# Performance work log

Hardware: AMD Instinct MI355X
Metric: run time of the kernel (lower is better)

## Reference

```python
import jax, jax.numpy as jnp
import numpy as np

EPS = 1e-6
B, N, K = 4, 65536, 16
D_IN, D_OUT, DH = 8, 16, 8  # DH = d_out // 2


def _bn(x, g, b):
    # train-mode BatchNorm2d over (B, N, K) per channel (channels-last here)
    m = jnp.mean(x, axis=(0, 1, 2))
    v = jnp.var(x, axis=(0, 1, 2))
    return (x - m) * jax.lax.rsqrt(v + EPS) * g + b


def _conv(x, w, b):
    # 1x1 Conv2d == per-point linear; x: (B,N,K,Cin), w: (Cout,Cin)
    return jnp.einsum('bnki,oi->bnko', x, w) + b


def _lse(coords, feats, idx, w, b, g, bt):
    # coords: (B,N,3), feats: (B,N,1,D), idx: (B,N,K)
    nbrs = jnp.take_along_axis(coords[:, :, None, :], idx[:, :, :, None], axis=1)  # (B,N,K,3)
    ctr = jnp.broadcast_to(coords[:, :, None, :], nbrs.shape)
    dist = jnp.ones(idx.shape + (1,), dtype=coords.dtype)  # torch path passes idx only -> dist = ones
    enc = jnp.concatenate([ctr, nbrs, ctr - nbrs, dist], axis=-1)  # (B,N,K,10)
    h = jax.nn.relu(_bn(_conv(enc, w, b), g, bt))
    f = jnp.broadcast_to(feats, idx.shape + (feats.shape[-1],))
    return jnp.concatenate([h, f], axis=-1)  # (B,N,K,2*D)


def _pool(x, sw, w, b, g, bt):
    # attentive pooling: softmax over neighbor axis K (axis=2)
    scores = jax.nn.softmax(jnp.einsum('bnki,oi->bnko', x, sw), axis=2)
    agg = jnp.sum(scores * x, axis=2, keepdims=True)  # (B,N,1,C)
    return jax.nn.relu(_bn(_conv(agg, w, b), g, bt))


def setup_inputs() -> dict:
    key = jax.random.key(0)
    ks = jax.random.split(key, 16)
    rn = lambda k, s: (0.1 * jax.random.normal(k, s)).astype(jnp.float32)
    inp = {
        'coords': jax.random.normal(ks[0], (B, N, 3), dtype=jnp.float32),
        'features': jax.random.normal(ks[1], (B, D_IN, N, 1), dtype=jnp.float32),
        'idx': jax.random.randint(ks[2], (B, N, K), 0, N, dtype=jnp.int32),
        # mlp1: d_in -> d_out//2, no bn, LeakyReLU(0.2)
        'w1': rn(ks[3], (DH, D_IN)), 'b1': jnp.zeros((DH,), jnp.float32),
        # lse1 mlp: 10 -> d_out//2, bn + ReLU
        'lse1_w': rn(ks[4], (DH, 10)), 'lse1_b': jnp.zeros((DH,), jnp.float32),
        'lse1_g': jnp.ones((DH,), jnp.float32), 'lse1_bt': jnp.zeros((DH,), jnp.float32),
        # pool1: in d_out -> out d_out//2
        'p1_sw': rn(ks[5], (D_OUT, D_OUT)),
        'p1_w': rn(ks[6], (DH, D_OUT)), 'p1_b': jnp.zeros((DH,), jnp.float32),
        'p1_g': jnp.ones((DH,), jnp.float32), 'p1_bt': jnp.zeros((DH,), jnp.float32),
        # lse2
        'lse2_w': rn(ks[7], (DH, 10)), 'lse2_b': jnp.zeros((DH,), jnp.float32),
        'lse2_g': jnp.ones((DH,), jnp.float32), 'lse2_bt': jnp.zeros((DH,), jnp.float32),
        # pool2: in d_out -> out d_out
        'p2_sw': rn(ks[8], (D_OUT, D_OUT)),
        'p2_w': rn(ks[9], (D_OUT, D_OUT)), 'p2_b': jnp.zeros((D_OUT,), jnp.float32),
        'p2_g': jnp.ones((D_OUT,), jnp.float32), 'p2_bt': jnp.zeros((D_OUT,), jnp.float32),
        # mlp2: d_out -> 2*d_out (no bn/act)
        'w2': rn(ks[10], (2 * D_OUT, D_OUT)), 'b2': jnp.zeros((2 * D_OUT,), jnp.float32),
        # shortcut: d_in -> 2*d_out, bn, no act
        'sc_w': rn(ks[11], (2 * D_OUT, D_IN)), 'sc_b': jnp.zeros((2 * D_OUT,), jnp.float32),
        'sc_g': jnp.ones((2 * D_OUT,), jnp.float32), 'sc_bt': jnp.zeros((2 * D_OUT,), jnp.float32),
    }
    return inp


def reference(coords, features, idx, w1, b1, lse1_w, lse1_b, lse1_g, lse1_bt,
              p1_sw, p1_w, p1_b, p1_g, p1_bt, lse2_w, lse2_b, lse2_g, lse2_bt,
              p2_sw, p2_w, p2_b, p2_g, p2_bt, w2, b2, sc_w, sc_b, sc_g, sc_bt):
    feats = jnp.transpose(features, (0, 2, 3, 1))  # (B,N,1,d_in) channels-last
    x = jax.nn.leaky_relu(_conv(feats, w1, b1), 0.2)           # (B,N,1,DH)
    x = _lse(coords, x, idx, lse1_w, lse1_b, lse1_g, lse1_bt)  # (B,N,K,D_OUT)
    x = _pool(x, p1_sw, p1_w, p1_b, p1_g, p1_bt)               # (B,N,1,DH)
    x = _lse(coords, x, idx, lse2_w, lse2_b, lse2_g, lse2_bt)  # (B,N,K,D_OUT)
    x = _pool(x, p2_sw, p2_w, p2_b, p2_g, p2_bt)               # (B,N,1,D_OUT)
    out = jax.nn.leaky_relu(
        _conv(x, w2, b2) + _bn(_conv(feats, sc_w, sc_b), sc_g, sc_bt), 0.01)
    return jnp.transpose(out, (0, 3, 1, 2))  # (B, 2*d_out, N, 1)
```

## Files before the change

kernel.cpp:

```cpp
#include <hip/hip_runtime.h>

#define NB 4
#define NN 65536
#define NK 16
#define NP (NB * NN)
#define BN_EPS 1e-6f
#define LOG2E 1.44269504088896f

#define WS_ENC_M   0
#define WS_SC_M    32
#define WS_S_Y2    96
#define WS_SS_Y2   104
#define WS_S_Y4    112
#define WS_SS_Y4   128
#define WS_Y2      1024
#define WS_Y4      (1024 + NP * 8)
#define WS_C4      (1024 + NP * 24)

template <int NCH>
__device__ inline void blockReduceAtomic(float (&v)[NCH], float* __restrict__ dst) {
    __shared__ float red[4][NCH];
    const int lane = threadIdx.x & 63;
    const int wv = threadIdx.x >> 6;
    __syncthreads();
#pragma unroll
    for (int c = 0; c < NCH; c++) {
        float x = v[c];
#pragma unroll
        for (int off = 32; off > 0; off >>= 1) x += __shfl_xor(x, off, 64);
        if (lane == 0) red[wv][c] = x;
    }
    __syncthreads();
    for (int c = threadIdx.x; c < NCH; c += 256)
        atomicAdd(dst + c, red[0][c] + red[1][c] + red[2][c] + red[3][c]);
    __syncthreads();
}

__device__ inline void bn_from_enc(const float* __restrict__ M, const float* __restrict__ w,
                                   float b, float g, float bt, float& sc, float& sh) {
    float u[6];
    u[0] = w[0] + w[6]; u[1] = w[1] + w[7]; u[2] = w[2] + w[8];
    u[3] = w[3] - w[6]; u[4] = w[4] - w[7]; u[5] = w[5] - w[8];
    const float beta = b + w[9];
    float lin = 0.f;
#pragma unroll
    for (int i = 0; i < 6; i++) lin += u[i] * M[i];
    float quad = u[0] * u[0] * M[6] + 2.f * u[0] * u[1] * M[7] + 2.f * u[0] * u[2] * M[8]
               + u[1] * u[1] * M[9] + 2.f * u[1] * u[2] * M[10] + u[2] * u[2] * M[11];
#pragma unroll
    for (int i = 0; i < 3; i++)
#pragma unroll
        for (int j = 0; j < 3; j++) quad += 2.f * u[i] * u[3 + j] * M[12 + i * 3 + j];
    quad += u[3] * u[3] * M[21] + 2.f * u[3] * u[4] * M[22] + 2.f * u[3] * u[5] * M[23]
          + u[4] * u[4] * M[24] + 2.f * u[4] * u[5] * M[25] + u[5] * u[5] * M[26];
    const float cnt = (float)NP * (float)NK;
    const float sum = lin + cnt * beta;
    const float ss = quad + 2.f * beta * lin + cnt * beta * beta;
    const float m = sum / cnt, v = ss / cnt - m * m;
    sc = g * rsqrtf(v + BN_EPS);
    sh = bt - m * sc;
}

__global__ __launch_bounds__(256) void k_prep(
    const float* __restrict__ coords, float4* __restrict__ c4) {
    const int p = blockIdx.x * 256 + threadIdx.x;
    c4[p] = make_float4(coords[3 * p], coords[3 * p + 1], coords[3 * p + 2], 0.f);
}

__global__ __launch_bounds__(256) void k_stats(
    const float4* __restrict__ c4, const float* __restrict__ feats,
    const int* __restrict__ idx, float* __restrict__ ws) {
    const int tid = threadIdx.x;
    const int p = blockIdx.x * 256 + tid;
    const int b = p >> 16;
    const int n = p & (NN - 1);

    {
        float accf[44];
        float f[8];
#pragma unroll
        for (int i = 0; i < 8; i++) f[i] = feats[(b * 8 + i) * NN + n];
#pragma unroll
        for (int i = 0; i < 8; i++) accf[i] = f[i];
        int t2 = 8;
#pragma unroll
        for (int i = 0; i < 8; i++)
#pragma unroll
            for (int j = i; j < 8; j++) accf[t2++] = f[i] * f[j];
        blockReduceAtomic<44>(accf, ws + WS_SC_M);
    }

    const int boff = b << 16;
    const float4 me = c4[p];
    const int4* ip = (const int4*)idx + p * 4;
    float sn0 = 0.f, sn1 = 0.f, sn2 = 0.f;
    float m00 = 0.f, m01 = 0.f, m02 = 0.f, m11 = 0.f, m12 = 0.f, m22 = 0.f;
#pragma unroll
    for (int q = 0; q < 4; q++) {
        int4 v = ip[q];
        int jj[4] = {v.x, v.y, v.z, v.w};
#pragma unroll
        for (int e = 0; e < 4; e++) {
            const float4 nn = c4[boff + jj[e]];
            sn0 += nn.x; sn1 += nn.y; sn2 += nn.z;
            m00 += nn.x * nn.x; m01 += nn.x * nn.y; m02 += nn.x * nn.z;
            m11 += nn.y * nn.y; m12 += nn.y * nn.z; m22 += nn.z * nn.z;
        }
    }
    float acc[27];
    acc[0] = 16.f * me.x; acc[1] = 16.f * me.y; acc[2] = 16.f * me.z;
    acc[3] = sn0; acc[4] = sn1; acc[5] = sn2;
    acc[6] = 16.f * me.x * me.x; acc[7] = 16.f * me.x * me.y; acc[8] = 16.f * me.x * me.z;
    acc[9] = 16.f * me.y * me.y; acc[10] = 16.f * me.y * me.z; acc[11] = 16.f * me.z * me.z;
    acc[12] = me.x * sn0; acc[13] = me.x * sn1; acc[14] = me.x * sn2;
    acc[15] = me.y * sn0; acc[16] = me.y * sn1; acc[17] = me.y * sn2;
    acc[18] = me.z * sn0; acc[19] = me.z * sn1; acc[20] = me.z * sn2;
    acc[21] = m00; acc[22] = m01; acc[23] = m02;
    acc[24] = m11; acc[25] = m12; acc[26] = m22;
    blockReduceAtomic<27>(acc, ws + WS_ENC_M);
}

__global__ __launch_bounds__(256) void k_pool1(
    const float4* __restrict__ c4, const float* __restrict__ feats,
    const int* __restrict__ idx,
    const float* __restrict__ w1, const float* __restrict__ b1,
    const float* __restrict__ lse1_w, const float* __restrict__ lse1_b,
    const float* __restrict__ lse1_g, const float* __restrict__ lse1_bt,
    const float* __restrict__ p1_sw, const float* __restrict__ p1_w,
    const float* __restrict__ p1_b, float* __restrict__ ws) {
    __shared__ float an[24], dc3[24], dcon[8], sws[64], pws[128], pbs[8], w1s[64], b1s[8];
    const int tid = threadIdx.x;
    if (tid < 8) {
        const int c = tid;
        const float* w = lse1_w + c * 10;
        float sc, sh;
        bn_from_enc(ws + WS_ENC_M, w, lse1_b[c], lse1_g[c], lse1_bt[c], sc, sh);
#pragma unroll
        for (int i = 0; i < 3; i++) {
            an[c * 3 + i] = sc * (w[3 + i] - w[6 + i]);
            dc3[c * 3 + i] = sc * (w[i] + w[6 + i]);
        }
        dcon[c] = sc * (lse1_b[c] + w[9]) + sh;
        b1s[c] = b1[c]; pbs[c] = p1_b[c];
    }
    if (tid < 64) {
        w1s[tid] = w1[tid];
        sws[tid] = p1_sw[(tid >> 3) * 16 + (tid & 7)] * LOG2E;
    }
    if (tid < 128) pws[tid] = p1_w[tid];
    __syncthreads();

    const int p = blockIdx.x * 256 + tid;
    const int b = p >> 16;
    const int n = p & (NN - 1);
    const int boff = b << 16;
    const float4 me = c4[p];
    float d[8];
#pragma unroll
    for (int c = 0; c < 8; c++)
        d[c] = dc3[c * 3] * me.x + dc3[c * 3 + 1] * me.y + dc3[c * 3 + 2] * me.z + dcon[c];
    const int4* ip = (const int4*)idx + p * 4;
    float l[8] = {}, ac[8] = {};
#pragma unroll
    for (int q = 0; q < 4; q++) {
        int4 v = ip[q];
        int jj[4] = {v.x, v.y, v.z, v.w};
#pragma unroll
        for (int e = 0; e < 4; e++) {
            const float4 nn = c4[boff + jj[e]];
            float h[8];
#pragma unroll
            for (int c = 0; c < 8; c++) {
                float y = an[c * 3] * nn.x + an[c * 3 + 1] * nn.y + an[c * 3 + 2] * nn.z + d[c];
                h[c] = y > 0.f ? y : 0.f;
            }
#pragma unroll
            for (int o = 0; o < 8; o++) {
                float s = 0.f;
#pragma unroll
                for (int i = 0; i < 8; i++) s += h[i] * sws[o * 8 + i];
                float e2 = exp2f(s);
                l[o] += e2; ac[o] += e2 * h[o];
            }
        }
    }
    float f[8];
#pragma unroll
    for (int i = 0; i < 8; i++) f[i] = feats[(b * 8 + i) * NN + n];
    float agg[16];
#pragma unroll
    for (int o = 0; o < 8; o++) agg[o] = ac[o] / l[o];
#pragma unroll
    for (int jq = 0; jq < 8; jq++) {
        float y = b1s[jq];
#pragma unroll
        for (int i = 0; i < 8; i++) y += f[i] * w1s[jq * 8 + i];
        agg[8 + jq] = y > 0.f ? y : 0.2f * y;
    }
    float st[16];
#pragma unroll
    for (int c = 0; c < 8; c++) {
        float y = pbs[c];
#pragma unroll
        for (int o = 0; o < 16; o++) y += agg[o] * pws[c * 16 + o];
        ws[WS_Y2 + c * NP + p] = y;
        st[c] = y; st[8 + c] = y * y;
    }
    blockReduceAtomic<16>(st, ws + WS_S_Y2);
}

__global__ __launch_bounds__(256) void k_pool2(
    const float4* __restrict__ c4, const int* __restrict__ idx,
    const float* __restrict__ lse2_w, const float* __restrict__ lse2_b,
    const float* __restrict__ lse2_g, const float* __restrict__ lse2_bt,
    const float* __restrict__ p1_g, const float* __restrict__ p1_bt,
    const float* __restrict__ p2_sw, const float* __restrict__ p2_w,
    const float* __restrict__ p2_b, float* __restrict__ ws) {
    __shared__ float an[24], dc3[24], dcon[8], p1sc[8], p1sh[8], sws[64], pws[256], pbs[16];
    const int tid = threadIdx.x;
    if (tid < 8) {
        const int c = tid;
        const float* w = lse2_w + c * 10;
        float sc, sh;
        bn_from_enc(ws + WS_ENC_M, w, lse2_b[c], lse2_g[c], lse2_bt[c], sc, sh);
#pragma unroll
        for (int i = 0; i < 3; i++) {
            an[c * 3 + i] = sc * (w[3 + i] - w[6 + i]);
            dc3[c * 3 + i] = sc * (w[i] + w[6 + i]);
        }
        dcon[c] = sc * (lse2_b[c] + w[9]) + sh;
    } else if (tid < 16) {
        const int c = tid - 8;
        const float cP = 1.f / (float)NP;
        float m = ws[WS_S_Y2 + c] * cP, vv = ws[WS_SS_Y2 + c] * cP - m * m;
        float sc = p1_g[c] * rsqrtf(vv + BN_EPS);
        p1sc[c] = sc; p1sh[c] = p1_bt[c] - m * sc;
    }
    if (tid < 64) sws[tid] = p2_sw[(tid >> 3) * 16 + (tid & 7)] * LOG2E;
    if (tid < 256) pws[tid] = p2_w[tid];
    if (tid < 16) pbs[tid] = p2_b[tid];
    __syncthreads();

    const int p = blockIdx.x * 256 + tid;
    const int boff = (p >> 16) << 16;
    const float4 me = c4[p];
    float d[8];
#pragma unroll
    for (int c = 0; c < 8; c++)
        d[c] = dc3[c * 3] * me.x + dc3[c * 3 + 1] * me.y + dc3[c * 3 + 2] * me.z + dcon[c];
    const int4* ip = (const int4*)idx + p * 4;
    float l[8] = {}, ac[8] = {};
#pragma unroll
    for (int q = 0; q < 4; q++) {
        int4 v = ip[q];
        int jj[4] = {v.x, v.y, v.z, v.w};
#pragma unroll
        for (int e = 0; e < 4; e++) {
            const float4 nn = c4[boff + jj[e]];
            float h[8];
#pragma unroll
            for (int c = 0; c < 8; c++) {
                float y = an[c * 3] * nn.x + an[c * 3 + 1] * nn.y + an[c * 3 + 2] * nn.z + d[c];
                h[c] = y > 0.f ? y : 0.f;
            }
#pragma unroll
            for (int o = 0; o < 8; o++) {
                float s = 0.f;
#pragma unroll
                for (int i = 0; i < 8; i++) s += h[i] * sws[o * 8 + i];
                float e2 = exp2f(s);
                l[o] += e2; ac[o] += e2 * h[o];
            }
        }
    }
    float agg[16];
#pragma unroll
    for (int o = 0; o < 8; o++) agg[o] = ac[o] / l[o];
#pragma unroll
    for (int c = 0; c < 8; c++) {
        float y = ws[WS_Y2 + c * NP + p] * p1sc[c] + p1sh[c];
        agg[8 + c] = y > 0.f ? y : 0.f;
    }
    float st[32];
#pragma unroll
    for (int c = 0; c < 16; c++) {
        float y = pbs[c];
#pragma unroll
        for (int o = 0; o < 16; o++) y += agg[o] * pws[c * 16 + o];
        ws[WS_Y4 + c * NP + p] = y;
        st[c] = y; st[16 + c] = y * y;
    }
    blockReduceAtomic<32>(st, ws + WS_S_Y4);
}

__global__ __launch_bounds__(256) void k_final(
    const float* __restrict__ feats, const float* __restrict__ w2,
    const float* __restrict__ b2, const float* __restrict__ sc_w,
    const float* __restrict__ sc_b, const float* __restrict__ p2_g,
    const float* __restrict__ p2_bt, const float* __restrict__ sc_g,
    const float* __restrict__ sc_bt, const float* __restrict__ ws,
    float* __restrict__ out) {
    __shared__ float w2s[512], b2s[32], scws[256], scbs[32],
        p2sc[16], p2sh[16], scsc[32], scsh[32];
    const int tid = threadIdx.x;
    for (int i = tid; i < 512; i += 256) w2s[i] = w2[i];
    if (tid < 256) scws[tid] = sc_w[tid];
    if (tid < 32) {
        b2s[tid] = b2[tid]; scbs[tid] = sc_b[tid];
        const int c = tid;
        const float* w = sc_w + c * 8;
        const float* S = ws + WS_SC_M;
        float lin = 0.f;
#pragma unroll
        for (int i = 0; i < 8; i++) lin += w[i] * S[i];
        float quad = 0.f;
        int t2 = 0;
#pragma unroll
        for (int i = 0; i < 8; i++)
#pragma unroll
            for (int j = i; j < 8; j++) {
                const float mm = S[8 + t2++];
                quad += (i == j ? 1.f : 2.f) * w[i] * w[j] * mm;
            }
        const float cnt = (float)NP;
        const float bb = sc_b[c];
        const float sum = lin + cnt * bb;
        const float ss = quad + 2.f * bb * lin + cnt * bb * bb;
        const float m = sum / cnt, vv = ss / cnt - m * m;
        const float sc = sc_g[c] * rsqrtf(vv + BN_EPS);
        scsc[c] = sc; scsh[c] = sc_bt[c] - m * sc;
    }
    if (tid < 16) {
        const int c = tid;
        const float cP = 1.f / (float)NP;
        float m = ws[WS_S_Y4 + c] * cP, vv = ws[WS_SS_Y4 + c] * cP - m * m;
        float sc = p2_g[c] * rsqrtf(vv + BN_EPS);
        p2sc[c] = sc; p2sh[c] = p2_bt[c] - m * sc;
    }
    __syncthreads();

    const int p = blockIdx.x * 256 + tid;
    const int b = p >> 16;
    const int n = p & (NN - 1);
    float x4[16];
#pragma unroll
    for (int c = 0; c < 16; c++) {
        float y = ws[WS_Y4 + c * NP + p] * p2sc[c] + p2sh[c];
        x4[c] = y > 0.f ? y : 0.f;
    }
    float f[8];
#pragma unroll
    for (int i = 0; i < 8; i++) f[i] = feats[(b * 8 + i) * NN + n];
#pragma unroll
    for (int c = 0; c < 32; c++) {
        float s = scbs[c];
#pragma unroll
        for (int i = 0; i < 8; i++) s += f[i] * scws[c * 8 + i];
        s = s * scsc[c] + scsh[c];
        float m = b2s[c];
#pragma unroll
        for (int o = 0; o < 16; o++) m += x4[o] * w2s[c * 16 + o];
        float vv = m + s;
        out[(b * 32 + c) * NN + n] = vv > 0.f ? vv : 0.01f * vv;
    }
}

extern "C" void kernel_launch(void* const* d_in, const int* in_sizes, int n_in,
                              void* d_out, int out_size, void* d_ws, size_t ws_size,
                              hipStream_t stream) {
    (void)in_sizes; (void)n_in; (void)out_size; (void)ws_size;
    const float* coords = (const float*)d_in[0];
    const float* features = (const float*)d_in[1];
    const int* idx = (const int*)d_in[2];
    const float* w1 = (const float*)d_in[3];
    const float* b1 = (const float*)d_in[4];
    const float* lse1_w = (const float*)d_in[5];
    const float* lse1_b = (const float*)d_in[6];
    const float* lse1_g = (const float*)d_in[7];
    const float* lse1_bt = (const float*)d_in[8];
    const float* p1_sw = (const float*)d_in[9];
    const float* p1_w = (const float*)d_in[10];
    const float* p1_b = (const float*)d_in[11];
    const float* p1_g = (const float*)d_in[12];
    const float* p1_bt = (const float*)d_in[13];
    const float* lse2_w = (const float*)d_in[14];
    const float* lse2_b = (const float*)d_in[15];
    const float* lse2_g = (const float*)d_in[16];
    const float* lse2_bt = (const float*)d_in[17];
    const float* p2_sw = (const float*)d_in[18];
    const float* p2_w = (const float*)d_in[19];
    const float* p2_b = (const float*)d_in[20];
    const float* p2_g = (const float*)d_in[21];
    const float* p2_bt = (const float*)d_in[22];
    const float* w2 = (const float*)d_in[23];
    const float* b2 = (const float*)d_in[24];
    const float* sc_w = (const float*)d_in[25];
    const float* sc_b = (const float*)d_in[26];
    const float* sc_g = (const float*)d_in[27];
    const float* sc_bt = (const float*)d_in[28];
    float* ws = (float*)d_ws;
    float* out = (float*)d_out;
    float4* c4 = (float4*)(ws + WS_C4);

    const int NBLK = NP / 256;
    hipMemsetAsync(ws, 0, 144 * sizeof(float), stream);
    k_prep<<<NBLK, 256, 0, stream>>>(coords, c4);
    k_stats<<<NBLK, 256, 0, stream>>>(c4, features, idx, ws);
    k_pool1<<<NBLK, 256, 0, stream>>>(c4, features, idx, w1, b1, lse1_w, lse1_b,
                                      lse1_g, lse1_bt, p1_sw, p1_w, p1_b, ws);
    k_pool2<<<NBLK, 256, 0, stream>>>(c4, idx, lse2_w, lse2_b, lse2_g, lse2_bt,
                                      p1_g, p1_bt, p2_sw, p2_w, p2_b, ws);
    k_final<<<NBLK, 256, 0, stream>>>(features, w2, b2, sc_w, sc_b, p2_g, p2_bt,
                                      sc_g, sc_bt, ws, out);
}
```

Baseline: 363.9 us.

## Fuse both LSE/pool gathers into one pass and fold prep into stats

```diff
diff --git a/kernel.cpp b/kernel.cpp
--- a/kernel.cpp
+++ b/kernel.cpp
@@ -61,15 +61,9 @@
     sh = bt - m * sc;
 }
 
-__global__ __launch_bounds__(256) void k_prep(
-    const float* __restrict__ coords, float4* __restrict__ c4) {
-    const int p = blockIdx.x * 256 + threadIdx.x;
-    c4[p] = make_float4(coords[3 * p], coords[3 * p + 1], coords[3 * p + 2], 0.f);
-}
-
 __global__ __launch_bounds__(256) void k_stats(
-    const float4* __restrict__ c4, const float* __restrict__ feats,
-    const int* __restrict__ idx, float* __restrict__ ws) {
+    const float* __restrict__ coords, const float* __restrict__ feats,
+    const int* __restrict__ idx, float4* __restrict__ c4, float* __restrict__ ws) {
     const int tid = threadIdx.x;
     const int p = blockIdx.x * 256 + tid;
     const int b = p >> 16;
@@ -90,31 +84,53 @@
         blockReduceAtomic<44>(accf, ws + WS_SC_M);
     }
 
-    const int boff = b << 16;
-    const float4 me = c4[p];
+    const float cx = coords[3 * p], cy = coords[3 * p + 1], cz = coords[3 * p + 2];
+    c4[p] = make_float4(cx, cy, cz, 0.f);
+    const float* cb = coords + b * NN * 3;
     const int4* ip = (const int4*)idx + p * 4;
     float sn0 = 0.f, sn1 = 0.f, sn2 = 0.f;
     float m00 = 0.f, m01 = 0.f, m02 = 0.f, m11 = 0.f, m12 = 0.f, m22 = 0.f;
-#pragma unroll
-    for (int q = 0; q < 4; q++) {
-        int4 v = ip[q];
-        int jj[4] = {v.x, v.y, v.z, v.w};
+
+    auto proc = [&](float nx, float ny, float nz) {
+        sn0 += nx; sn1 += ny; sn2 += nz;
+        m00 += nx * nx; m01 += nx * ny; m02 += nx * nz;
+        m11 += ny * ny; m12 += ny * nz; m22 += nz * nz;
+    };
+
+    int4 v0 = ip[0];
+    float ax[4], ay[4], az[4];
+    {
+        int jj[4] = {v0.x, v0.y, v0.z, v0.w};
 #pragma unroll
         for (int e = 0; e < 4; e++) {
-            const float4 nn = c4[boff + jj[e]];
-            sn0 += nn.x; sn1 += nn.y; sn2 += nn.z;
-            m00 += nn.x * nn.x; m01 += nn.x * nn.y; m02 += nn.x * nn.z;
-            m11 += nn.y * nn.y; m12 += nn.y * nn.z; m22 += nn.z * nn.z;
-        }
-    }
+            ax[e] = cb[3 * jj[e]]; ay[e] = cb[3 * jj[e] + 1]; az[e] = cb[3 * jj[e] + 2];
+        }
+    }
+#pragma unroll 1
+    for (int q = 0; q < 3; q++) {
+        const int4 vn = ip[q + 1];
+        int jj[4] = {vn.x, vn.y, vn.z, vn.w};
+        float tx[4], ty[4], tz[4];
+#pragma unroll
+        for (int e = 0; e < 4; e++) {
+            tx[e] = cb[3 * jj[e]]; ty[e] = cb[3 * jj[e] + 1]; tz[e] = cb[3 * jj[e] + 2];
+        }
+#pragma unroll
+        for (int e = 0; e < 4; e++) proc(ax[e], ay[e], az[e]);
+#pragma unroll
+        for (int e = 0; e < 4; e++) { ax[e] = tx[e]; ay[e] = ty[e]; az[e] = tz[e]; }
+    }
+#pragma unroll
+    for (int e = 0; e < 4; e++) proc(ax[e], ay[e], az[e]);
+
     float acc[27];
-    acc[0] = 16.f * me.x; acc[1] = 16.f * me.y; acc[2] = 16.f * me.z;
+    acc[0] = 16.f * cx; acc[1] = 16.f * cy; acc[2] = 16.f * cz;
     acc[3] = sn0; acc[4] = sn1; acc[5] = sn2;
-    acc[6] = 16.f * me.x * me.x; acc[7] = 16.f * me.x * me.y; acc[8] = 16.f * me.x * me.z;
-    acc[9] = 16.f * me.y * me.y; acc[10] = 16.f * me.y * me.z; acc[11] = 16.f * me.z * me.z;
-    acc[12] = me.x * sn0; acc[13] = me.x * sn1; acc[14] = me.x * sn2;
-    acc[15] = me.y * sn0; acc[16] = me.y * sn1; acc[17] = me.y * sn2;
-    acc[18] = me.z * sn0; acc[19] = me.z * sn1; acc[20] = me.z * sn2;
+    acc[6] = 16.f * cx * cx; acc[7] = 16.f * cx * cy; acc[8] = 16.f * cx * cz;
+    acc[9] = 16.f * cy * cy; acc[10] = 16.f * cy * cz; acc[11] = 16.f * cz * cz;
+    acc[12] = cx * sn0; acc[13] = cx * sn1; acc[14] = cx * sn2;
+    acc[15] = cy * sn0; acc[16] = cy * sn1; acc[17] = cy * sn2;
+    acc[18] = cz * sn0; acc[19] = cz * sn1; acc[20] = cz * sn2;
     acc[21] = m00; acc[22] = m01; acc[23] = m02;
     acc[24] = m11; acc[25] = m12; acc[26] = m22;
     blockReduceAtomic<27>(acc, ws + WS_ENC_M);
@@ -126,28 +142,49 @@
     const float* __restrict__ w1, const float* __restrict__ b1,
     const float* __restrict__ lse1_w, const float* __restrict__ lse1_b,
     const float* __restrict__ lse1_g, const float* __restrict__ lse1_bt,
+    const float* __restrict__ lse2_w, const float* __restrict__ lse2_b,
+    const float* __restrict__ lse2_g, const float* __restrict__ lse2_bt,
     const float* __restrict__ p1_sw, const float* __restrict__ p1_w,
-    const float* __restrict__ p1_b, float* __restrict__ ws) {
-    __shared__ float an[24], dc3[24], dcon[8], sws[64], pws[128], pbs[8], w1s[64], b1s[8];
+    const float* __restrict__ p1_b,
+    const float* __restrict__ p2_sw, const float* __restrict__ p2_w,
+    const float* __restrict__ p2_b, float* __restrict__ ws) {
+    __shared__ float an1[24], dcA[24], dkA[8], an2[24], dcB[24], dkB[8],
+        sws1[64], sws2[64], pws1[128], pws2[256], pbs1[8], pbs2[16], w1s[64], b1s[8];
     const int tid = threadIdx.x;
     if (tid < 8) {
         const int c = tid;
-        const float* w = lse1_w + c * 10;
-        float sc, sh;
-        bn_from_enc(ws + WS_ENC_M, w, lse1_b[c], lse1_g[c], lse1_bt[c], sc, sh);
-#pragma unroll
-        for (int i = 0; i < 3; i++) {
-            an[c * 3 + i] = sc * (w[3 + i] - w[6 + i]);
-            dc3[c * 3 + i] = sc * (w[i] + w[6 + i]);
-        }
-        dcon[c] = sc * (lse1_b[c] + w[9]) + sh;
-        b1s[c] = b1[c]; pbs[c] = p1_b[c];
-    }
+        {
+            const float* w = lse1_w + c * 10;
+            float sc, sh;
+            bn_from_enc(ws + WS_ENC_M, w, lse1_b[c], lse1_g[c], lse1_bt[c], sc, sh);
+#pragma unroll
+            for (int i = 0; i < 3; i++) {
+                an1[c * 3 + i] = sc * (w[3 + i] - w[6 + i]);
+                dcA[c * 3 + i] = sc * (w[i] + w[6 + i]);
+            }
+            dkA[c] = sc * (lse1_b[c] + w[9]) + sh;
+        }
+        {
+            const float* w = lse2_w + c * 10;
+            float sc, sh;
+            bn_from_enc(ws + WS_ENC_M, w, lse2_b[c], lse2_g[c], lse2_bt[c], sc, sh);
+#pragma unroll
+            for (int i = 0; i < 3; i++) {
+                an2[c * 3 + i] = sc * (w[3 + i] - w[6 + i]);
+                dcB[c * 3 + i] = sc * (w[i] + w[6 + i]);
+            }
+            dkB[c] = sc * (lse2_b[c] + w[9]) + sh;
+        }
+        b1s[c] = b1[c]; pbs1[c] = p1_b[c];
+    }
+    if (tid < 16) pbs2[tid] = p2_b[tid];
     if (tid < 64) {
         w1s[tid] = w1[tid];
-        sws[tid] = p1_sw[(tid >> 3) * 16 + (tid & 7)] * LOG2E;
-    }
-    if (tid < 128) pws[tid] = p1_w[tid];
+        sws1[tid] = p1_sw[(tid >> 3) * 16 + (tid & 7)] * LOG2E;
+        sws2[tid] = p2_sw[(tid >> 3) * 16 + (tid & 7)] * LOG2E;
+    }
+    if (tid < 128) pws1[tid] = p1_w[tid];
+    if (tid < 256) pws2[tid] = p2_w[tid];
     __syncthreads();
 
     const int p = blockIdx.x * 256 + tid;
@@ -155,41 +192,63 @@
     const int n = p & (NN - 1);
     const int boff = b << 16;
     const float4 me = c4[p];
-    float d[8];
-#pragma unroll
-    for (int c = 0; c < 8; c++)
-        d[c] = dc3[c * 3] * me.x + dc3[c * 3 + 1] * me.y + dc3[c * 3 + 2] * me.z + dcon[c];
+    float d1[8], d2[8];
+#pragma unroll
+    for (int c = 0; c < 8; c++) {
+        d1[c] = dcA[c * 3] * me.x + dcA[c * 3 + 1] * me.y + dcA[c * 3 + 2] * me.z + dkA[c];
+        d2[c] = dcB[c * 3] * me.x + dcB[c * 3 + 1] * me.y + dcB[c * 3 + 2] * me.z + dkB[c];
+    }
     const int4* ip = (const int4*)idx + p * 4;
-    float l[8] = {}, ac[8] = {};
-#pragma unroll
-    for (int q = 0; q < 4; q++) {
-        int4 v = ip[q];
-        int jj[4] = {v.x, v.y, v.z, v.w};
-#pragma unroll
-        for (int e = 0; e < 4; e++) {
-            const float4 nn = c4[boff + jj[e]];
-            float h[8];
-#pragma unroll
-            for (int c = 0; c < 8; c++) {
-                float y = an[c * 3] * nn.x + an[c * 3 + 1] * nn.y + an[c * 3 + 2] * nn.z + d[c];
-                h[c] = y > 0.f ? y : 0.f;
-            }
-#pragma unroll
-            for (int o = 0; o < 8; o++) {
-                float s = 0.f;
-#pragma unroll
-                for (int i = 0; i < 8; i++) s += h[i] * sws[o * 8 + i];
-                float e2 = exp2f(s);
-                l[o] += e2; ac[o] += e2 * h[o];
-            }
-        }
-    }
+    float l1[8] = {}, a1[8] = {}, l2[8] = {}, a2[8] = {};
+
+    auto proc = [&](const float4 nn) {
+        float h[8];
+#pragma unroll
+        for (int c = 0; c < 8; c++) {
+            float y = an1[c * 3] * nn.x + an1[c * 3 + 1] * nn.y + an1[c * 3 + 2] * nn.z + d1[c];
+            h[c] = y > 0.f ? y : 0.f;
+        }
+#pragma unroll
+        for (int o = 0; o < 8; o++) {
+            float s = 0.f;
+#pragma unroll
+            for (int i = 0; i < 8; i++) s += h[i] * sws1[o * 8 + i];
+            float e2 = exp2f(s);
+            l1[o] += e2; a1[o] += e2 * h[o];
+        }
+#pragma unroll
+        for (int c = 0; c < 8; c++) {
+            float y = an2[c * 3] * nn.x + an2[c * 3 + 1] * nn.y + an2[c * 3 + 2] * nn.z + d2[c];
+            h[c] = y > 0.f ? y : 0.f;
+        }
+#pragma unroll
+        for (int o = 0; o < 8; o++) {
+            float s = 0.f;
+#pragma unroll
+            for (int i = 0; i < 8; i++) s += h[i] * sws2[o * 8 + i];
+            float e2 = exp2f(s);
+            l2[o] += e2; a2[o] += e2 * h[o];
+        }
+    };
+
+    int4 v = ip[0];
+    float4 n0 = c4[boff + v.x], n1 = c4[boff + v.y], n2 = c4[boff + v.z], n3 = c4[boff + v.w];
+#pragma unroll 1
+    for (int q = 0; q < 3; q++) {
+        const int4 vn = ip[q + 1];
+        const float4 t0 = c4[boff + vn.x], t1 = c4[boff + vn.y],
+                     t2 = c4[boff + vn.z], t3 = c4[boff + vn.w];
+        proc(n0); proc(n1); proc(n2); proc(n3);
+        n0 = t0; n1 = t1; n2 = t2; n3 = t3;
+    }
+    proc(n0); proc(n1); proc(n2); proc(n3);
+
     float f[8];
 #pragma unroll
     for (int i = 0; i < 8; i++) f[i] = feats[(b * 8 + i) * NN + n];
     float agg[16];
 #pragma unroll
-    for (int o = 0; o < 8; o++) agg[o] = ac[o] / l[o];
+    for (int o = 0; o < 8; o++) agg[o] = a1[o] * __builtin_amdgcn_rcpf(l1[o]);
 #pragma unroll
     for (int jq = 0; jq < 8; jq++) {
         float y = b1s[jq];
@@ -200,93 +259,53 @@
     float st[16];
 #pragma unroll
     for (int c = 0; c < 8; c++) {
-        float y = pbs[c];
-#pragma unroll
-        for (int o = 0; o < 16; o++) y += agg[o] * pws[c * 16 + o];
+        float y = pbs1[c];
+#pragma unroll
+        for (int o = 0; o < 16; o++) y += agg[o] * pws1[c * 16 + o];
         ws[WS_Y2 + c * NP + p] = y;
         st[c] = y; st[8 + c] = y * y;
     }
+    float g2[8];
+#pragma unroll
+    for (int o = 0; o < 8; o++) g2[o] = a2[o] * __builtin_amdgcn_rcpf(l2[o]);
+#pragma unroll
+    for (int c = 0; c < 16; c++) {
+        float y = pbs2[c];
+#pragma unroll
+        for (int o = 0; o < 8; o++) y += g2[o] * pws2[c * 16 + o];
+        ws[WS_Y4 + c * NP + p] = y;
+    }
     blockReduceAtomic<16>(st, ws + WS_S_Y2);
 }
 
-__global__ __launch_bounds__(256) void k_pool2(
-    const float4* __restrict__ c4, const int* __restrict__ idx,
-    const float* __restrict__ lse2_w, const float* __restrict__ lse2_b,
-    const float* __restrict__ lse2_g, const float* __restrict__ lse2_bt,
+__global__ __launch_bounds__(256) void k_pool2e(
     const float* __restrict__ p1_g, const float* __restrict__ p1_bt,
-    const float* __restrict__ p2_sw, const float* __restrict__ p2_w,
-    const float* __restrict__ p2_b, float* __restrict__ ws) {
-    __shared__ float an[24], dc3[24], dcon[8], p1sc[8], p1sh[8], sws[64], pws[256], pbs[16];
+    const float* __restrict__ p2_w, float* __restrict__ ws) {
+    __shared__ float p1sc[8], p1sh[8], pwsb[128];
     const int tid = threadIdx.x;
     if (tid < 8) {
         const int c = tid;
-        const float* w = lse2_w + c * 10;
-        float sc, sh;
-        bn_from_enc(ws + WS_ENC_M, w, lse2_b[c], lse2_g[c], lse2_bt[c], sc, sh);
-#pragma unroll
-        for (int i = 0; i < 3; i++) {
-            an[c * 3 + i] = sc * (w[3 + i] - w[6 + i]);
-            dc3[c * 3 + i] = sc * (w[i] + w[6 + i]);
-        }
-        dcon[c] = sc * (lse2_b[c] + w[9]) + sh;
-    } else if (tid < 16) {
-        const int c = tid - 8;
         const float cP = 1.f / (float)NP;
         float m = ws[WS_S_Y2 + c] * cP, vv = ws[WS_SS_Y2 + c] * cP - m * m;
         float sc = p1_g[c] * rsqrtf(vv + BN_EPS);
         p1sc[c] = sc; p1sh[c] = p1_bt[c] - m * sc;
     }
-    if (tid < 64) sws[tid] = p2_sw[(tid >> 3) * 16 + (tid & 7)] * LOG2E;
-    if (tid < 256) pws[tid] = p2_w[tid];
-    if (tid < 16) pbs[tid] = p2_b[tid];
+    if (tid < 128) pwsb[tid] = p2_w[(tid >> 3) * 16 + 8 + (tid & 7)];
     __syncthreads();
 
     const int p = blockIdx.x * 256 + tid;
-    const int boff = (p >> 16) << 16;
-    const float4 me = c4[p];
-    float d[8];
-#pragma unroll
-    for (int c = 0; c < 8; c++)
-        d[c] = dc3[c * 3] * me.x + dc3[c * 3 + 1] * me.y + dc3[c * 3 + 2] * me.z + dcon[c];
-    const int4* ip = (const int4*)idx + p * 4;
-    float l[8] = {}, ac[8] = {};
-#pragma unroll
-    for (int q = 0; q < 4; q++) {
-        int4 v = ip[q];
-        int jj[4] = {v.x, v.y, v.z, v.w};
-#pragma unroll
-        for (int e = 0; e < 4; e++) {
-            const float4 nn = c4[boff + jj[e]];
-            float h[8];
-#pragma unroll
-            for (int c = 0; c < 8; c++) {
-                float y = an[c * 3] * nn.x + an[c * 3 + 1] * nn.y + an[c * 3 + 2] * nn.z + d[c];
-                h[c] = y > 0.f ? y : 0.f;
-            }
-#pragma unroll
-            for (int o = 0; o < 8; o++) {
-                float s = 0.f;
-#pragma unroll
-                for (int i = 0; i < 8; i++) s += h[i] * sws[o * 8 + i];
-                float e2 = exp2f(s);
-                l[o] += e2; ac[o] += e2 * h[o];
-            }
-        }
-    }
-    float agg[16];
-#pragma unroll
-    for (int o = 0; o < 8; o++) agg[o] = ac[o] / l[o];
+    float x2[8];
 #pragma unroll
     for (int c = 0; c < 8; c++) {
         float y = ws[WS_Y2 + c * NP + p] * p1sc[c] + p1sh[c];
-        agg[8 + c] = y > 0.f ? y : 0.f;
+        x2[c] = y > 0.f ? y : 0.f;
     }
     float st[32];
 #pragma unroll
     for (int c = 0; c < 16; c++) {
-        float y = pbs[c];
-#pragma unroll
-        for (int o = 0; o < 16; o++) y += agg[o] * pws[c * 16 + o];
+        float y = ws[WS_Y4 + c * NP + p];
+#pragma unroll
+        for (int o = 0; o < 8; o++) y += x2[o] * pwsb[c * 8 + o];
         ws[WS_Y4 + c * NP + p] = y;
         st[c] = y; st[16 + c] = y * y;
     }
@@ -403,13 +422,13 @@
     float4* c4 = (float4*)(ws + WS_C4);
 
     const int NBLK = NP / 256;
-    hipMemsetAsync(ws, 0, 144 * sizeof(float), stream);
-    k_prep<<<NBLK, 256, 0, stream>>>(coords, c4);
-    k_stats<<<NBLK, 256, 0, stream>>>(c4, features, idx, ws);
-    k_pool1<<<NBLK, 256, 0, stream>>>(c4, features, idx, w1, b1, lse1_w, lse1_b,
-                                      lse1_g, lse1_bt, p1_sw, p1_w, p1_b, ws);
-    k_pool2<<<NBLK, 256, 0, stream>>>(c4, idx, lse2_w, lse2_b, lse2_g, lse2_bt,
-                                      p1_g, p1_bt, p2_sw, p2_w, p2_b, ws);
+    (void)hipMemsetAsync(ws, 0, 144 * sizeof(float), stream);
+    k_stats<<<NBLK, 256, 0, stream>>>(coords, features, idx, c4, ws);
+    k_pool1<<<NBLK, 256, 0, stream>>>(c4, features, idx, w1, b1,
+                                      lse1_w, lse1_b, lse1_g, lse1_bt,
+                                      lse2_w, lse2_b, lse2_g, lse2_bt,
+                                      p1_sw, p1_w, p1_b, p2_sw, p2_w, p2_b, ws);
+    k_pool2e<<<NBLK, 256, 0, stream>>>(p1_g, p1_bt, p2_w, ws);
     k_final<<<NBLK, 256, 0, stream>>>(features, w2, b2, sc_w, sc_b, p2_g, p2_bt,
                                       sc_g, sc_bt, ws, out);
 }
```

New measurement: 332.7 us. -8.6%, faster.
